# Kernel optimization log

Measured on AMD Instinct MI355X. Metric: run time of the kernel, lower is better.

Reference implementation:

```python
import jax, jax.numpy as jnp
import numpy as np

GRID = (8, 8)
B, C, H, W = 16, 256, 64, 64
N_NETS = GRID[0] * GRID[1]
EPS = 1e-5  # torch BatchNorm2d default


def _region_index():
    # Faithful to the original code: networks[i * j + j] == networks[j*(i+1)]
    gh, gw = GRID
    i = np.arange(gh)[:, None]
    j = np.arange(gw)[None, :]
    return (i * j + j).reshape(-1)  # [gh*gw] int indices into the 64 networks


def setup_inputs() -> dict:
    key = jax.random.key(0)
    ks = jax.random.split(key, 7)
    x = jax.random.normal(ks[0], (B, C, H, W), jnp.float32)
    gamma = 1.0 + 0.1 * jax.random.normal(ks[1], (N_NETS, C), jnp.float32)
    beta = 0.1 * jax.random.normal(ks[2], (N_NETS, C), jnp.float32)
    mean = 0.1 * jax.random.normal(ks[3], (N_NETS, C), jnp.float32)
    var = jax.random.uniform(ks[4], (N_NETS, C), jnp.float32, minval=0.5, maxval=1.5)
    conv_w = 0.05 * jax.random.normal(ks[5], (N_NETS, C, C, 3, 3), jnp.float32)
    conv_b = 0.01 * jax.random.normal(ks[6], (N_NETS, C), jnp.float32)
    return dict(x=x, gamma=gamma, beta=beta, mean=mean, var=var,
                conv_w=conv_w, conv_b=conv_b)


def reference(x, gamma, beta, mean, var, conv_w, conv_b):
    gh, gw = GRID
    b, c, h, w = x.shape
    ph, pw = h // gh, w // gw
    # [B,C,H,W] -> [gh*gw, B, C, ph, pw]
    xp = (x.reshape(b, c, gh, ph, gw, pw)
           .transpose(2, 4, 0, 1, 3, 5)
           .reshape(gh * gw, b, c, ph, pw))

    idx = jnp.asarray(_region_index())
    g, bt, m, v = gamma[idx], beta[idx], mean[idx], var[idx]
    wk, cb = conv_w[idx], conv_b[idx]

    def region(xi, gi, bi, mi, vi, wi, cbi):
        # inference-mode BatchNorm2d
        scale = (gi * jax.lax.rsqrt(vi + EPS))[None, :, None, None]
        hh = (xi - mi[None, :, None, None]) * scale + bi[None, :, None, None]
        hh = jax.nn.relu(hh)
        y = jax.lax.conv_general_dilated(
            hh, wi, window_strides=(1, 1), padding=((1, 1), (1, 1)),
            dimension_numbers=('NCHW', 'OIHW', 'NCHW'))
        return y + cbi[None, :, None, None] + xi  # residual add

    yp = jax.vmap(region)(xp, g, bt, m, v, wk, cb)  # [gh*gw, B, C, ph, pw]
    y = (yp.reshape(gh, gw, b, c, ph, pw)
           .transpose(2, 3, 0, 4, 1, 5)
           .reshape(b, c, h, w))
    return y
```

## Files before the change

kernel.cpp:

```cpp
#include <hip/hip_runtime.h>
#include <hip/hip_bf16.h>
#include <stdint.h>


typedef __attribute__((ext_vector_type(8))) short bf16x8;
typedef __attribute__((ext_vector_type(4))) float f32x4;

typedef const __attribute__((address_space(1))) unsigned int gu32;
typedef __attribute__((address_space(3))) unsigned int lu32;

__device__ __forceinline__ void g2l16(const void* g, void* l) {
  __builtin_amdgcn_global_load_lds((gu32*)g, (lu32*)l, 16, 0, 0);
}

__global__ void wtrans_kernel(const float* __restrict__ w,
                              __hip_bfloat16* __restrict__ wb) {
  const int co  = blockIdx.x;
  const int net = blockIdx.y;
  const int ci  = threadIdx.x;
  const float* src = w + (size_t)((net * 256 + co) * 256 + ci) * 9;
#pragma unroll
  for (int t = 0; t < 9; ++t) {
    wb[(size_t)((net * 9 + t) * 256 + co) * 256 + ci] = __float2bfloat16(src[t]);
  }
}

__global__ void bnrelu_kernel(const float* __restrict__ x,
                              const float* __restrict__ gamma,
                              const float* __restrict__ beta,
                              const float* __restrict__ mean,
                              const float* __restrict__ var,
                              __hip_bfloat16* __restrict__ hh) {
  const int blk = blockIdx.x;
  const int reg = blk >> 4, b = blk & 15;
  const int gi = reg >> 3, gj = reg & 7;
  const int net = gj * (gi + 1);
  const int tid = threadIdx.x;

  __shared__ float sc[256], sh[256];
  __shared__ float tile[64 * 65];

  {
    float g = gamma[net * 256 + tid];
    float bt = beta[net * 256 + tid];
    float m = mean[net * 256 + tid];
    float v = var[net * 256 + tid];
    float s = g * rsqrtf(v + 1e-5f);
    sc[tid] = s;
    sh[tid] = bt - m * s;
  }
  __syncthreads();

  const float* xb = x + (size_t)b * 256 * 4096 + (gi * 8) * 64 + gj * 8;
  __hip_bfloat16* hb = hh + (size_t)(reg * 16 + b) * 64 * 256;

  const int px = tid & 63, cl0 = tid >> 6;
  const int yy = px >> 3, xx = px & 7;
  const int wcl = tid & 63, wpx0 = tid >> 6;

  for (int cc = 0; cc < 4; ++cc) {
    const int c0 = cc * 64;
#pragma unroll
    for (int i = 0; i < 16; ++i) {
      int cl = cl0 + i * 4;
      int c = c0 + cl;
      float v = xb[(size_t)c * 4096 + yy * 64 + xx];
      float h = v * sc[c] + sh[c];
      tile[px * 65 + cl] = fmaxf(h, 0.f);
    }
    __syncthreads();
#pragma unroll
    for (int i = 0; i < 16; ++i) {
      int p = wpx0 + i * 4;
      hb[p * 256 + c0 + wcl] = __float2bfloat16(tile[p * 65 + wcl]);
    }
    __syncthreads();
  }
}

__global__ __launch_bounds__(256, 2) void conv_kernel(
    const __hip_bfloat16* __restrict__ hh,
    const __hip_bfloat16* __restrict__ wb,
    const float* __restrict__ xin,
    const float* __restrict__ cbias,
    float* __restrict__ outp) {
  __shared__ __align__(16) char sA[16384];
  __shared__ __align__(16) char sB[16384];

  const int bx = blockIdx.x;
  const int r = bx >> 4;
  const int mt = bx & 7;
  const int nt = (bx >> 3) & 1;
  const int gi = r >> 3, gj = r & 7;
  const int net = gj * (gi + 1);

  const int tid = threadIdx.x;
  const int lane = tid & 63;
  const int wv = tid >> 6;
  const int wm = (wv & 1) * 64;
  const int wn = (wv >> 1) * 64;
  const int ln = lane & 15;
  const int q = lane >> 4;

  const __hip_bfloat16* Aslab = hh + (size_t)(r * 16 + mt * 2) * (64 * 256);
  const __hip_bfloat16* Bbase =
      wb + (size_t)(net * 9) * (256 * 256) + (size_t)(nt * 128) * 256;

  int bl[4], py[4], pxr[4];
#pragma unroll
  for (int mf = 0; mf < 4; ++mf) {
    int m = wm + mf * 16 + ln;
    bl[mf] = m >> 6;
    py[mf] = (m >> 3) & 7;
    pxr[mf] = m & 7;
  }
  int boff[4][2];
#pragma unroll
  for (int nf = 0; nf < 4; ++nf) {
    int nrow = wn + nf * 16 + ln;
#pragma unroll
    for (int kk = 0; kk < 2; ++kk) {
      int sl = kk * 4 + q;
      int sp = (sl + (nrow & 7)) & 7;
      boff[nf][kk] = nrow * 128 + sp * 16;
    }
  }

  f32x4 acc[4][4];
#pragma unroll
  for (int mf = 0; mf < 4; ++mf)
#pragma unroll
    for (int nf = 0; nf < 4; ++nf)
      acc[mf][nf] = (f32x4){0.f, 0.f, 0.f, 0.f};

  const bf16x8 zero8 = {0, 0, 0, 0, 0, 0, 0, 0};

#pragma unroll 1
  for (int cc = 0; cc < 4; ++cc) {
    const int c0 = cc * 64;
#pragma unroll
    for (int i = 0; i < 4; ++i) {
      int slot = i * 256 + tid;
      int row = slot >> 3, sp = slot & 7;
      int sl = (sp - (row & 7)) & 7;
      g2l16(Aslab + (size_t)row * 256 + c0 + sl * 8, sA + slot * 16);
    }
#pragma unroll
    for (int tap = 0; tap < 9; ++tap) {
      const int dy = tap / 3 - 1, dx = tap % 3 - 1;
      const __hip_bfloat16* Btap = Bbase + (size_t)tap * (256 * 256);
#pragma unroll
      for (int i = 0; i < 4; ++i) {
        int slot = i * 256 + tid;
        int row = slot >> 3, sp = slot & 7;
        int sl = (sp - (row & 7)) & 7;
        g2l16(Btap + (size_t)row * 256 + c0 + sl * 8, sB + slot * 16);
      }
      __syncthreads();

      int arow[4], avalid[4];
#pragma unroll
      for (int mf = 0; mf < 4; ++mf) {
        int sy = py[mf] + dy, sx = pxr[mf] + dx;
        int v = ((unsigned)sy < 8u) & ((unsigned)sx < 8u);
        avalid[mf] = v;
        arow[mf] = (bl[mf] << 6) + (v ? (sy * 8 + sx) : 0);
      }
#pragma unroll
      for (int kk = 0; kk < 2; ++kk) {
        bf16x8 afr[4], bfr[4];
#pragma unroll
        for (int mf = 0; mf < 4; ++mf) {
          int row = arow[mf];
          int sp = ((kk * 4 + q) + (row & 7)) & 7;
          bf16x8 v = *(const bf16x8*)(sA + row * 128 + sp * 16);
          afr[mf] = avalid[mf] ? v : zero8;
        }
#pragma unroll
        for (int nf = 0; nf < 4; ++nf)
          bfr[nf] = *(const bf16x8*)(sB + boff[nf][kk]);
#pragma unroll
        for (int mf = 0; mf < 4; ++mf)
#pragma unroll
          for (int nf = 0; nf < 4; ++nf)
            acc[mf][nf] = __builtin_amdgcn_mfma_f32_16x16x32_bf16(
                afr[mf], bfr[nf], acc[mf][nf], 0, 0, 0);
      }
      __syncthreads();
    }
  }

  const int nbase = nt * 128 + wn;
#pragma unroll
  for (int nf = 0; nf < 4; ++nf) {
    const int n = nbase + nf * 16 + ln;
    const float cb = cbias[net * 256 + n];
#pragma unroll
    for (int mf = 0; mf < 4; ++mf) {
      int mloc = wm + mf * 16 + q * 4;
      int b = mt * 2 + (mloc >> 6);
      int px = mloc & 63;
      int yy = px >> 3, x0 = px & 7;
      size_t off =
          (((size_t)b * 256 + n) * 64 + (gi * 8 + yy)) * 64 + (gj * 8 + x0);
      f32x4 res = *(const f32x4*)(xin + off);
      f32x4 o = acc[mf][nf];
      o = o + res;
      o = o + cb;
      *(f32x4*)(outp + off) = o;
    }
  }
}

extern "C" void kernel_launch(void* const* d_in, const int* in_sizes, int n_in,
                              void* d_out, int out_size, void* d_ws,
                              size_t ws_size, hipStream_t stream) {
  const float* x      = (const float*)d_in[0];
  const float* gamma  = (const float*)d_in[1];
  const float* beta   = (const float*)d_in[2];
  const float* mean   = (const float*)d_in[3];
  const float* var    = (const float*)d_in[4];
  const float* conv_w = (const float*)d_in[5];
  const float* conv_b = (const float*)d_in[6];
  float* out = (float*)d_out;

  __hip_bfloat16* wb = (__hip_bfloat16*)d_ws;
  __hip_bfloat16* hh = (__hip_bfloat16*)((char*)d_ws + 75497472);

  wtrans_kernel<<<dim3(256, 64), 256, 0, stream>>>(conv_w, wb);
  bnrelu_kernel<<<1024, 256, 0, stream>>>(x, gamma, beta, mean, var, hh);
  conv_kernel<<<1024, 256, 0, stream>>>(hh, wb, x, conv_b, out);
}
```

Measured before the change: 417.2 us.

## Stage full A slab in LDS, load weights directly, vectorize transpose kernels

The conv kernel now loads the whole 128x256 activation slab into LDS once, with a zero row for padding, and drops the per-tap LDS staging of weights and its barriers. B fragments are read straight from global memory into registers. The weight-transpose and BN-ReLU kernels are rewritten to use LDS tiles with swizzling and 16-byte vectorized stores instead of scalar bf16 writes. The risks are lower occupancy from 66KB of LDS per block and extra global-load latency on the weight path with no buffering.

Result: slower. 479.6 us (+14.9%).

```diff
diff --git a/kernel.cpp b/kernel.cpp
--- a/kernel.cpp
+++ b/kernel.cpp
@@ -13,15 +13,50 @@
   __builtin_amdgcn_global_load_lds((gu32*)g, (lu32*)l, 16, 0, 0);
 }
 
+__device__ __forceinline__ unsigned short f2bf(float f) {
+  union { __hip_bfloat16 h; unsigned short u; } cv;
+  cv.h = __float2bfloat16(f);
+  return cv.u;
+}
+
 __global__ void wtrans_kernel(const float* __restrict__ w,
                               __hip_bfloat16* __restrict__ wb) {
-  const int co  = blockIdx.x;
+  const int co8 = blockIdx.x;
   const int net = blockIdx.y;
-  const int ci  = threadIdx.x;
-  const float* src = w + (size_t)((net * 256 + co) * 256 + ci) * 9;
-#pragma unroll
-  for (int t = 0; t < 9; ++t) {
-    wb[(size_t)((net * 9 + t) * 256 + co) * 256 + ci] = __float2bfloat16(src[t]);
+  const int tid = threadIdx.x;
+  __shared__ __align__(16) unsigned short t[9 * 8 * 256];
+
+  const int cip = tid & 127;
+  const int ch  = tid >> 7;
+  const int ci0 = cip * 2;
+
+#pragma unroll
+  for (int cl = 0; cl < 4; ++cl) {
+    const int col = ch * 4 + cl;
+    const int co = co8 * 8 + col;
+    const float* src = w + ((size_t)(net * 256 + co) * 256 + ci0) * 9;
+    float a[18];
+#pragma unroll
+    for (int i = 0; i < 18; ++i) a[i] = src[i];
+#pragma unroll
+    for (int tap = 0; tap < 9; ++tap) {
+      unsigned int pk = (unsigned)f2bf(a[tap]) | ((unsigned)f2bf(a[tap + 9]) << 16);
+      *(unsigned int*)&t[tap * 2048 + col * 256 + ci0] = pk;
+    }
+  }
+  __syncthreads();
+
+  __hip_bfloat16* base = wb + (size_t)net * 589824;
+#pragma unroll
+  for (int k = 0; k < 9; ++k) {
+    int ck = k * 256 + tid;
+    int tap = ck >> 8;
+    int col = (ck >> 5) & 7;
+    int cr = ck & 31;
+    bf16x8 v = *(const bf16x8*)&t[tap * 2048 + col * 256 + cr * 8];
+    unsigned short* dst = (unsigned short*)base +
+        ((size_t)tap * 256 + co8 * 8 + col) * 256 + cr * 8;
+    *(bf16x8*)dst = v;
   }
 }
 
@@ -38,7 +73,7 @@
   const int tid = threadIdx.x;
 
   __shared__ float sc[256], sh[256];
-  __shared__ float tile[64 * 65];
+  __shared__ __align__(16) unsigned short tile[64 * 256];
 
   {
     float g = gamma[net * 256 + tid];
@@ -51,30 +86,35 @@
   }
   __syncthreads();
 
-  const float* xb = x + (size_t)b * 256 * 4096 + (gi * 8) * 64 + gj * 8;
-  __hip_bfloat16* hb = hh + (size_t)(reg * 16 + b) * 64 * 256;
-
-  const int px = tid & 63, cl0 = tid >> 6;
+  const float* xb = x + (size_t)b * 1048576 + (gi * 8) * 64 + gj * 8;
+  const int px = tid & 63, cw = tid >> 6;
   const int yy = px >> 3, xx = px & 7;
-  const int wcl = tid & 63, wpx0 = tid >> 6;
-
-  for (int cc = 0; cc < 4; ++cc) {
-    const int c0 = cc * 64;
-#pragma unroll
-    for (int i = 0; i < 16; ++i) {
-      int cl = cl0 + i * 4;
-      int c = c0 + cl;
-      float v = xb[(size_t)c * 4096 + yy * 64 + xx];
-      float h = v * sc[c] + sh[c];
-      tile[px * 65 + cl] = fmaxf(h, 0.f);
-    }
-    __syncthreads();
-#pragma unroll
-    for (int i = 0; i < 16; ++i) {
-      int p = wpx0 + i * 4;
-      hb[p * 256 + c0 + wcl] = __float2bfloat16(tile[p * 65 + wcl]);
-    }
-    __syncthreads();
+
+#pragma unroll
+  for (int j = 0; j < 8; ++j) {
+    const int chunk = cw * 8 + j;
+    const int c0 = chunk * 8;
+    bf16x8 v;
+#pragma unroll
+    for (int e = 0; e < 8; ++e) {
+      int c = c0 + e;
+      float tv = xb[(size_t)c * 4096 + yy * 64 + xx];
+      tv = fmaxf(tv * sc[c] + sh[c], 0.f);
+      v[e] = (short)f2bf(tv);
+    }
+    int phys = (chunk + px) & 31;
+    *(bf16x8*)&tile[px * 256 + phys * 8] = v;
+  }
+  __syncthreads();
+
+  unsigned short* hb = (unsigned short*)(hh + (size_t)(reg * 16 + b) * 16384);
+#pragma unroll
+  for (int k = 0; k < 8; ++k) {
+    int ck = k * 256 + tid;
+    int p = ck >> 5, cl = ck & 31;
+    int phys = (cl + p) & 31;
+    bf16x8 v = *(const bf16x8*)&tile[p * 256 + phys * 8];
+    *(bf16x8*)(hb + p * 256 + cl * 8) = v;
   }
 }
 
@@ -84,8 +124,7 @@
     const float* __restrict__ xin,
     const float* __restrict__ cbias,
     float* __restrict__ outp) {
-  __shared__ __align__(16) char sA[16384];
-  __shared__ __align__(16) char sB[16384];
+  __shared__ __align__(16) char sA[66048];
 
   const int bx = blockIdx.x;
   const int r = bx >> 4;
@@ -103,8 +142,19 @@
   const int q = lane >> 4;
 
   const __hip_bfloat16* Aslab = hh + (size_t)(r * 16 + mt * 2) * (64 * 256);
-  const __hip_bfloat16* Bbase =
-      wb + (size_t)(net * 9) * (256 * 256) + (size_t)(nt * 128) * 256;
+
+#pragma unroll
+  for (int i = 0; i < 16; ++i) {
+    int s = i * 256 + tid;
+    int row = s >> 5, sp = s & 31;
+    int cl = (sp & 24) | (((sp & 7) - row) & 7);
+    g2l16(Aslab + (size_t)row * 256 + cl * 8, sA + s * 16);
+  }
+  if (tid < 32) *(f32x4*)(sA + 65536 + tid * 16) = (f32x4){0.f, 0.f, 0.f, 0.f};
+  __syncthreads();
+
+  const unsigned short* Bl = (const unsigned short*)wb +
+      (size_t)net * 589824 + (size_t)(nt * 128 + wn + ln) * 256 + q * 8;
 
   int bl[4], py[4], pxr[4];
 #pragma unroll
@@ -114,17 +164,6 @@
     py[mf] = (m >> 3) & 7;
     pxr[mf] = m & 7;
   }
-  int boff[4][2];
-#pragma unroll
-  for (int nf = 0; nf < 4; ++nf) {
-    int nrow = wn + nf * 16 + ln;
-#pragma unroll
-    for (int kk = 0; kk < 2; ++kk) {
-      int sl = kk * 4 + q;
-      int sp = (sl + (nrow & 7)) & 7;
-      boff[nf][kk] = nrow * 128 + sp * 16;
-    }
-  }
 
   f32x4 acc[4][4];
 #pragma unroll
@@ -133,60 +172,41 @@
     for (int nf = 0; nf < 4; ++nf)
       acc[mf][nf] = (f32x4){0.f, 0.f, 0.f, 0.f};
 
-  const bf16x8 zero8 = {0, 0, 0, 0, 0, 0, 0, 0};
-
 #pragma unroll 1
   for (int cc = 0; cc < 4; ++cc) {
-    const int c0 = cc * 64;
-#pragma unroll
-    for (int i = 0; i < 4; ++i) {
-      int slot = i * 256 + tid;
-      int row = slot >> 3, sp = slot & 7;
-      int sl = (sp - (row & 7)) & 7;
-      g2l16(Aslab + (size_t)row * 256 + c0 + sl * 8, sA + slot * 16);
-    }
 #pragma unroll
     for (int tap = 0; tap < 9; ++tap) {
       const int dy = tap / 3 - 1, dx = tap % 3 - 1;
-      const __hip_bfloat16* Btap = Bbase + (size_t)tap * (256 * 256);
-#pragma unroll
-      for (int i = 0; i < 4; ++i) {
-        int slot = i * 256 + tid;
-        int row = slot >> 3, sp = slot & 7;
-        int sl = (sp - (row & 7)) & 7;
-        g2l16(Btap + (size_t)row * 256 + c0 + sl * 8, sB + slot * 16);
-      }
-      __syncthreads();
-
-      int arow[4], avalid[4];
+      bf16x8 bfr[4][2];
+#pragma unroll
+      for (int nf = 0; nf < 4; ++nf)
+#pragma unroll
+        for (int kk = 0; kk < 2; ++kk)
+          bfr[nf][kk] = *(const bf16x8*)(Bl + (size_t)tap * 65536 +
+                                         nf * 4096 + cc * 64 + kk * 32);
+      int arow[4];
 #pragma unroll
       for (int mf = 0; mf < 4; ++mf) {
         int sy = py[mf] + dy, sx = pxr[mf] + dx;
-        int v = ((unsigned)sy < 8u) & ((unsigned)sx < 8u);
-        avalid[mf] = v;
-        arow[mf] = (bl[mf] << 6) + (v ? (sy * 8 + sx) : 0);
+        bool v = ((unsigned)sy < 8u) & ((unsigned)sx < 8u);
+        arow[mf] = v ? (bl[mf] * 64 + sy * 8 + sx) : 128;
       }
 #pragma unroll
       for (int kk = 0; kk < 2; ++kk) {
-        bf16x8 afr[4], bfr[4];
+        bf16x8 afr[4];
 #pragma unroll
         for (int mf = 0; mf < 4; ++mf) {
           int row = arow[mf];
-          int sp = ((kk * 4 + q) + (row & 7)) & 7;
-          bf16x8 v = *(const bf16x8*)(sA + row * 128 + sp * 16);
-          afr[mf] = avalid[mf] ? v : zero8;
+          int phys = cc * 8 + ((kk * 4 + q + row) & 7);
+          afr[mf] = *(const bf16x8*)(sA + row * 512 + phys * 16);
         }
-#pragma unroll
-        for (int nf = 0; nf < 4; ++nf)
-          bfr[nf] = *(const bf16x8*)(sB + boff[nf][kk]);
 #pragma unroll
         for (int mf = 0; mf < 4; ++mf)
 #pragma unroll
           for (int nf = 0; nf < 4; ++nf)
             acc[mf][nf] = __builtin_amdgcn_mfma_f32_16x16x32_bf16(
-                afr[mf], bfr[nf], acc[mf][nf], 0, 0, 0);
+                afr[mf], bfr[nf][kk], acc[mf][nf], 0, 0, 0);
       }
-      __syncthreads();
     }
   }
 
@@ -227,7 +247,7 @@
   __hip_bfloat16* wb = (__hip_bfloat16*)d_ws;
   __hip_bfloat16* hh = (__hip_bfloat16*)((char*)d_ws + 75497472);
 
-  wtrans_kernel<<<dim3(256, 64), 256, 0, stream>>>(conv_w, wb);
+  wtrans_kernel<<<dim3(32, 64), 256, 0, stream>>>(conv_w, wb);
   bnrelu_kernel<<<1024, 256, 0, stream>>>(x, gamma, beta, mean, var, hh);
   conv_kernel<<<1024, 256, 0, stream>>>(hh, wb, x, conv_b, out);
 }
```
